# Kernel optimization log

Hardware: AMD Instinct MI355X
Metric: run time of the kernel (lower is better)

The kernel has to match this reference:

```python
import jax, jax.numpy as jnp
from jax import lax
import numpy as np

NUM_CENTROIDS = 1024
RADIUS = 0.5
K = 32
EPS = 1e-5


def _fps(xyz, num_samples):
    """Farthest point sampling. Deterministic start at index 0 (torch uses randint)."""
    B, N, _ = xyz.shape

    def step(carry, _):
        distances, farthest = carry
        centroid = jnp.take_along_axis(xyz, farthest[:, None, None], axis=1)  # [B,1,3]
        d = jnp.sum((xyz - centroid) ** 2, axis=-1)  # [B,N]
        distances = jnp.minimum(distances, d)
        nxt = jnp.argmax(distances, axis=-1).astype(jnp.int32)
        return (distances, nxt), farthest

    init = (jnp.full((B, N), jnp.inf, dtype=xyz.dtype), jnp.zeros((B,), jnp.int32))
    _, idxs = lax.scan(step, init, None, length=num_samples)  # [M,B]
    return jnp.transpose(idxs)  # [B,M]


def _ball_query(xyz, new_xyz):
    """K nearest neighbors within RADIUS; out-of-ball slots fall back to nearest."""
    d2 = (jnp.sum(new_xyz ** 2, -1)[:, :, None] + jnp.sum(xyz ** 2, -1)[:, None, :]
          - 2.0 * jnp.einsum('bmd,bnd->bmn', new_xyz, xyz))
    dist = jnp.sqrt(jnp.maximum(d2, 0.0))  # [B,M,N] cdist
    dist = jnp.where(dist > RADIUS, jnp.inf, dist)
    neg_vals, idx = lax.top_k(-dist, K)  # smallest-K distances
    mask = jnp.isinf(neg_vals)  # outside radius
    idx = jnp.where(mask, idx[:, :, 0:1], idx)
    return idx  # [B,M,K]


def _forward(xyz, features, Ws, bs, gs, bts):
    B, N, _ = xyz.shape
    cidx = lax.stop_gradient(_fps(xyz, NUM_CENTROIDS))  # [B,M] int
    new_xyz = jnp.take_along_axis(xyz, cidx[:, :, None], axis=1)  # [B,M,3]
    gidx = lax.stop_gradient(_ball_query(xyz, new_xyz))  # [B,M,K] int
    flat = gidx.reshape(B, -1)
    gxyz = jnp.take_along_axis(xyz, flat[:, :, None], axis=1).reshape(B, NUM_CENTROIDS, K, 3)
    gxyz = gxyz - new_xyz[:, :, None, :]
    gfeat = jnp.take_along_axis(features, flat[:, :, None], axis=1).reshape(B, NUM_CENTROIDS, K, -1)
    h = jnp.concatenate([gxyz, gfeat], axis=-1)  # [B,M,K,C+3]
    for W, b, g, bt in zip(Ws, bs, gs, bts):
        # 1x1 Conv1d == per-point linear over channels
        h = jnp.einsum('bmkc,oc->bmko', h, W) + b
        # BatchNorm1d in training mode: batch stats over (B*M, K), biased var
        mu = jnp.mean(h, axis=(0, 1, 2))
        var = jnp.var(h, axis=(0, 1, 2))
        h = (h - mu) * lax.rsqrt(var + EPS) * g + bt
        h = jax.nn.gelu(h, approximate=False)  # torch nn.GELU default (exact erf)
    return new_xyz, jnp.max(h, axis=2)  # [B,M,3], [B,M,128]


def setup_inputs() -> dict:
    key = jax.random.key(0)
    ks = jax.random.split(key, 8)
    B, N, C = 8, 8192, 64
    xyz = jax.random.normal(ks[0], (B, N, 3), jnp.float32)
    features = jax.random.normal(ks[1], (B, N, C), jnp.float32)
    chans = [C + 3, 64, 64, 128]
    inp = {"xyz": xyz, "features": features}
    for l in range(3):
        cin, cout = chans[l], chans[l + 1]
        inp[f"W{l + 1}"] = jax.random.normal(ks[2 + l], (cout, cin), jnp.float32) / jnp.float32(np.sqrt(cin))
        inp[f"b{l + 1}"] = jnp.zeros((cout,), jnp.float32)
        inp[f"g{l + 1}"] = jnp.ones((cout,), jnp.float32)
        inp[f"bt{l + 1}"] = jnp.zeros((cout,), jnp.float32)
    return inp


def reference(xyz, features, W1, b1, g1, bt1, W2, b2, g2, bt2, W3, b3, g3, bt3):
    return _forward(xyz, features, (W1, W2, W3), (b1, b2, b3), (g1, g2, g3), (bt1, bt2, bt3))
```

## Files before the change

### kernel.cpp

```cpp
#include <hip/hip_runtime.h>
#include <cstdint>
#include <cstddef>

#define BATCH 8
#define NPTS  8192
#define MCENT 1024
#define KNN   32
#define CFEAT 64
#define EPS_F 1e-5f

#define WS_NEED 73400320ull

__device__ __forceinline__ float erf_fast(float x) {
  float a = fabsf(x);
  float t = __builtin_amdgcn_rcpf(fmaf(0.3275911f, a, 1.0f));
  float p = fmaf(1.061405429f, t, -1.453152027f);
  p = fmaf(p, t, 1.421413741f);
  p = fmaf(p, t, -0.284496736f);
  p = fmaf(p, t, 0.254829592f);
  float e = __expf(-a * a);
  float y = fmaf(-p * t, e, 1.0f);
  return copysignf(y, x);
}
__device__ __forceinline__ float gelu_f(float x) {
  return 0.5f * x * (1.0f + erf_fast(x * 0.70710678118654752440f));
}

template<int CTRL>
__device__ __forceinline__ float dpp_max_step(float v) {
  int s = __builtin_amdgcn_update_dpp(__float_as_int(v), __float_as_int(v),
                                      CTRL, 0xf, 0xf, false);
  return fmaxf(v, __int_as_float(s));
}
__device__ __forceinline__ float wave_max_dpp(float v) {
  v = dpp_max_step<0x111>(v);
  v = dpp_max_step<0x112>(v);
  v = dpp_max_step<0x114>(v);
  v = dpp_max_step<0x118>(v);
  v = dpp_max_step<0x142>(v);
  v = dpp_max_step<0x143>(v);
  return v;
}
template<int CTRL>
__device__ __forceinline__ unsigned long long dpp_min64_step(unsigned long long v) {
  int lo = __builtin_amdgcn_update_dpp((int)(unsigned)(v & 0xffffffffull),
                                       (int)(unsigned)(v & 0xffffffffull),
                                       CTRL, 0xf, 0xf, false);
  int hi = __builtin_amdgcn_update_dpp((int)(unsigned)(v >> 32),
                                       (int)(unsigned)(v >> 32),
                                       CTRL, 0xf, 0xf, false);
  unsigned long long o = (((unsigned long long)(unsigned)hi) << 32) | (unsigned)lo;
  return o < v ? o : v;
}
__device__ __forceinline__ unsigned long long wave_min64_dpp(unsigned long long v) {
  v = dpp_min64_step<0x111>(v);
  v = dpp_min64_step<0x112>(v);
  v = dpp_min64_step<0x114>(v);
  v = dpp_min64_step<0x118>(v);
  v = dpp_min64_step<0x142>(v);
  v = dpp_min64_step<0x143>(v);
  return v;
}

template<int M, int HALF>
__device__ __forceinline__ void tree_step(float* s_, float* q_, int lane) {
  bool up = (lane & M) != 0;
#pragma unroll
  for (int j = 0; j < HALF; ++j) {
    float ks = up ? s_[j+HALF] : s_[j];
    float ds = up ? s_[j]      : s_[j+HALF];
    s_[j] = ks + __shfl_xor(ds, M, 64);
    float kq = up ? q_[j+HALF] : q_[j];
    float dq = up ? q_[j]      : q_[j+HALF];
    q_[j] = kq + __shfl_xor(dq, M, 64);
  }
}
template<int M, int HALF>
__device__ __forceinline__ void ptree_step(float* g_, int kbit) {
  bool up = (kbit & M) != 0;
#pragma unroll
  for (int j = 0; j < HALF; ++j) {
    float kv = up ? g_[j+HALF] : g_[j];
    float dv = up ? g_[j]      : g_[j+HALF];
    g_[j] = fmaxf(kv, __shfl_xor(dv, M, 64));
  }
}

#define FPS_STEPS 64
#define BQCAP 512
__global__ __launch_bounds__(512, 1) void mega_kernel(
    const float* __restrict__ xyz, float* __restrict__ new_xyz,
    float* __restrict__ dist_ws, float* __restrict__ cst, int s0,
    int* __restrict__ gidx, const float* __restrict__ feats,
    const float* __restrict__ W1, const float* __restrict__ b1v,
    float* __restrict__ h1, float* __restrict__ part)
{
  __shared__ float pts[NPTS * 3];
  __shared__ float outb[FPS_STEPS * 3];
  __shared__ unsigned long long keys[2][8];
  __shared__ unsigned long long list[8][BQCAP];
  __shared__ float ls[512], lss[512];
  int blk = blockIdx.x, t = threadIdx.x;

  if (blk < 8) {
    if (s0 >= MCENT) return;
    int b = blk;
    const float* xb = xyz + (size_t)b * NPTS * 3;
    float px[16], py[16], pz[16], dist[16];
    {
      const float4* src = (const float4*)(xb + (size_t)t * 48);
      float4 buf[12];
#pragma unroll
      for (int i = 0; i < 12; ++i) buf[i] = src[i];
      const float* f = (const float*)buf;
#pragma unroll
      for (int i = 0; i < 16; ++i) {
        px[i] = f[i*3+0]; py[i] = f[i*3+1]; pz[i] = f[i*3+2];
      }
      float4* dst = (float4*)(pts + (size_t)t * 48);
#pragma unroll
      for (int i = 0; i < 12; ++i) dst[i] = buf[i];
    }
    float* dw = dist_ws + (size_t)b * NPTS + (size_t)t * 16;
    float cx, cy, cz;
    if (s0 == 0) {
#pragma unroll
      for (int i = 0; i < 16; ++i) dist[i] = __builtin_inff();
      cx = xb[0]; cy = xb[1]; cz = xb[2];
    } else {
      float4 d0 = *(const float4*)(dw + 0);
      float4 d1 = *(const float4*)(dw + 4);
      float4 d2 = *(const float4*)(dw + 8);
      float4 d3 = *(const float4*)(dw + 12);
      dist[0]=d0.x; dist[1]=d0.y; dist[2]=d0.z; dist[3]=d0.w;
      dist[4]=d1.x; dist[5]=d1.y; dist[6]=d1.z; dist[7]=d1.w;
      dist[8]=d2.x; dist[9]=d2.y; dist[10]=d2.z; dist[11]=d2.w;
      dist[12]=d3.x; dist[13]=d3.y; dist[14]=d3.z; dist[15]=d3.w;
      cx = cst[b*3+0]; cy = cst[b*3+1]; cz = cst[b*3+2];
    }
    int lane = t & 63, wv = t >> 6;

    for (int s = 0; s < FPS_STEPS; ++s) {
      if (t == 0) { outb[s*3+0] = cx; outb[s*3+1] = cy; outb[s*3+2] = cz; }
      float bd = -1.0f; int bslot = 0;
#pragma unroll
      for (int i = 0; i < 16; ++i) {
        float dx = __fsub_rn(px[i], cx);
        float dy = __fsub_rn(py[i], cy);
        float dz = __fsub_rn(pz[i], cz);
        float d  = __fadd_rn(__fadd_rn(__fmul_rn(dx,dx), __fmul_rn(dy,dy)), __fmul_rn(dz,dz));
        float nd = fminf(dist[i], d);
        dist[i] = nd;
        if (nd > bd) { bd = nd; bslot = i; }
      }
      float w = wave_max_dpp(bd);
      float wmax = __int_as_float(__builtin_amdgcn_readlane(__float_as_int(w), 63));
      unsigned long long mk = __ballot(bd == wmax);
      int sl = __ffsll((long long)mk) - 1;
      int widx = __builtin_amdgcn_readlane(t * 16 + bslot, sl);
      if (lane == 0)
        keys[s & 1][wv] = (((unsigned long long)__float_as_uint(wmax)) << 32)
                          | (unsigned)(8191 - widx);
      __syncthreads();
      unsigned long long bk = keys[s & 1][0];
#pragma unroll
      for (int w2 = 1; w2 < 8; ++w2) {
        unsigned long long o = keys[s & 1][w2];
        if (o > bk) bk = o;
      }
      int idx = 8191 - (int)(unsigned)(bk & 0xffffffffull);
      cx = pts[idx*3+0]; cy = pts[idx*3+1]; cz = pts[idx*3+2];
    }

    *(float4*)(dw + 0)  = make_float4(dist[0], dist[1], dist[2], dist[3]);
    *(float4*)(dw + 4)  = make_float4(dist[4], dist[5], dist[6], dist[7]);
    *(float4*)(dw + 8)  = make_float4(dist[8], dist[9], dist[10], dist[11]);
    *(float4*)(dw + 12) = make_float4(dist[12], dist[13], dist[14], dist[15]);
    if (t == 0) { cst[b*3+0] = cx; cst[b*3+1] = cy; cst[b*3+2] = cz; }
    __syncthreads();
    float* ob = new_xyz + (size_t)b * MCENT * 3 + (size_t)s0 * 3;
    for (int i = t; i < FPS_STEPS * 3; i += 512) ob[i] = outb[i];

  } else if (blk < 72) {
    int ph = s0 - FPS_STEPS;
    if (ph < 0 || ph >= MCENT) return;
    int wv = t >> 6, lane = t & 63;
    int c  = (blk - 8) * 8 + wv;
    int b  = c >> 6;
    int ci = ph + (c & 63);
    int gm = b * MCENT + ci;
    const float* cc = new_xyz + (size_t)gm * 3;
    float c0 = cc[0], c1 = cc[1], c2 = cc[2];
    float sc = __fadd_rn(__fadd_rn(__fmul_rn(c0,c0), __fmul_rn(c1,c1)), __fmul_rn(c2,c2));
    const float* xb = xyz + (size_t)b * NPTS * 3;

    unsigned cnt = 0;
    for (int j0 = 0; j0 < NPTS; j0 += 64) {
      int j = j0 + lane;
      float x = xb[j*3+0], y = xb[j*3+1], z = xb[j*3+2];
      float sx  = __fadd_rn(__fadd_rn(__fmul_rn(x,x), __fmul_rn(y,y)), __fmul_rn(z,z));
      float dot = __fadd_rn(__fadd_rn(__fmul_rn(c0,x), __fmul_rn(c1,y)), __fmul_rn(c2,z));
      float d2  = __fsub_rn(__fadd_rn(sc, sx), __fmul_rn(2.0f, dot));
      float dist = sqrtf(fmaxf(d2, 0.0f));
      bool in_ = (dist <= 0.5f);
      unsigned long long mask = __ballot(in_);
      unsigned off = (unsigned)__popcll(mask & ((1ull << lane) - 1ull));
      if (in_) {
        unsigned pos = cnt + off;
        if (pos < BQCAP)
          list[wv][pos] = (((unsigned long long)__float_as_uint(dist)) << 32) | (unsigned)j;
      }
      cnt += (unsigned)__popcll(mask);
    }
    if (cnt > BQCAP) cnt = BQCAP;

    unsigned long long e[8];
#pragma unroll
    for (int i = 0; i < 8; ++i) {
      unsigned pos = (unsigned)lane + ((unsigned)i << 6);
      e[i] = (pos < cnt) ? list[wv][pos] : ~0ull;
    }
#define CE_(a_, b_) { bool sw = e[b_] < e[a_]; \
                      unsigned long long lo_ = sw ? e[b_] : e[a_]; \
                      unsigned long long hi_ = sw ? e[a_] : e[b_]; \
                      e[a_] = lo_; e[b_] = hi_; }
    CE_(0,1) CE_(2,3) CE_(4,5) CE_(6,7)
    CE_(0,2) CE_(1,3) CE_(4,6) CE_(5,7)
    CE_(1,2) CE_(5,6)
    CE_(0,4) CE_(1,5) CE_(2,6) CE_(3,7)
    CE_(2,4) CE_(3,5)
    CE_(1,2) CE_(3,4) CE_(5,6)
#undef CE_

    int* gout = gidx + (size_t)gm * KNN;
    int first = 0;
    int kmax = (cnt < (unsigned)KNN) ? (int)cnt : KNN;
    for (int k = 0; k < KNN; ++k) {
      if (k < kmax) {
        unsigned long long wr = wave_min64_dpp(e[0]);
        unsigned lo32 = (unsigned)__builtin_amdgcn_readlane((int)(unsigned)(wr & 0xffffffffull), 63);
        unsigned hi32 = (unsigned)__builtin_amdgcn_readlane((int)(unsigned)(wr >> 32), 63);
        unsigned long long wmin = (((unsigned long long)hi32) << 32) | lo32;
        int idxv = (int)lo32;
        if (k == 0) first = idxv;
        if (lane == 0) gout[k] = idxv;
        bool win = (e[0] == wmin);
#pragma unroll
        for (int i = 0; i < 7; ++i) e[i] = win ? e[i+1] : e[i];
        e[7] = win ? ~0ull : e[7];
      } else {
        if (lane == 0) gout[k] = first;
      }
    }

  } else if (blk < 104) {
    int ph = s0 - 2 * FPS_STEPS;
    if (ph < 0 || ph >= MCENT) return;
    int row = (blk - 72) * 512 + t;
    int c   = row >> 5;
    int k   = row & 31;
    int b   = c >> 6;
    int ci  = ph + (c & 63);
    int p   = b * (MCENT * KNN) + ci * KNN + k;
    int idx = gidx[p];
    const float* cc = new_xyz + (size_t)(b * MCENT + ci) * 3;
    const float* q  = xyz + (size_t)(b * NPTS + idx) * 3;
    float in[67];
    in[0] = q[0] - cc[0];
    in[1] = q[1] - cc[1];
    in[2] = q[2] - cc[2];
    const float* fr = feats + (size_t)(b * NPTS + idx) * CFEAT;
#pragma unroll
    for (int j = 0; j < 64; j += 4) {
      float4 v = *(const float4*)(fr + j);
      in[3+j] = v.x; in[4+j] = v.y; in[5+j] = v.z; in[6+j] = v.w;
    }
    float* orow = h1 + (size_t)p * 64;
    for (int o4 = 0; o4 < 16; ++o4) {
      const float* w0 = W1 + (size_t)(o4 * 4) * 67;
      float a0 = b1v[o4*4+0], a1 = b1v[o4*4+1], a2 = b1v[o4*4+2], a3 = b1v[o4*4+3];
#pragma unroll
      for (int j = 0; j < 67; ++j) {
        float x = in[j];
        a0 = fmaf(x, w0[j],       a0);
        a1 = fmaf(x, w0[67+j],    a1);
        a2 = fmaf(x, w0[134+j],   a2);
        a3 = fmaf(x, w0[201+j],   a3);
      }
      *(float4*)(orow + o4*4) = make_float4(a0, a1, a2, a3);
    }

  } else {
    int ph = s0 - 3 * FPS_STEPS;
    if (ph < 0 || ph >= MCENT) return;
    int sb = blk - 104;
    int b  = sb >> 2;
    int rb = (sb & 3) * 512;
    int c  = t & 63, g = t >> 6;
    size_t base = (size_t)b * (MCENT * KNN) + (size_t)ph * KNN + rb;
    float s = 0.0f, ss = 0.0f;
    for (int r = g; r < 512; r += 8) {
      float v = h1[(base + r) * 64 + c];
      s += v;
      ss = fmaf(v, v, ss);
    }
    ls[t] = s; lss[t] = ss;
    __syncthreads();
    if (g == 0) {
#pragma unroll
      for (int gg = 1; gg < 8; ++gg) { s += ls[gg*64 + c]; ss += lss[gg*64 + c]; }
      int pblk = (ph >> 6) * 32 + sb;
      part[(size_t)pblk * 128 + c]      = s;
      part[(size_t)pblk * 128 + 64 + c] = ss;
    }
  }
}

__global__ __launch_bounds__(256) void l2_kernel(
    float* __restrict__ h, const float* __restrict__ W,
    const float* __restrict__ bv, const float* __restrict__ bnp,
    const float* __restrict__ btp)
{
  int p = blockIdx.x * 256 + threadIdx.x;
  float* row = h + (size_t)p * 64;
  float in[64];
#pragma unroll
  for (int j = 0; j < 64; j += 4) {
    float4 v = *(const float4*)(row + j);
    in[j+0] = gelu_f((v.x - bnp[j+0]) * bnp[64+j+0] + btp[j+0]);
    in[j+1] = gelu_f((v.y - bnp[j+1]) * bnp[64+j+1] + btp[j+1]);
    in[j+2] = gelu_f((v.z - bnp[j+2]) * bnp[64+j+2] + btp[j+2]);
    in[j+3] = gelu_f((v.w - bnp[j+3]) * bnp[64+j+3] + btp[j+3]);
  }
  for (int o4 = 0; o4 < 16; ++o4) {
    const float* w0 = W + (size_t)(o4 * 4) * 64;
    float a0 = bv[o4*4+0], a1 = bv[o4*4+1], a2 = bv[o4*4+2], a3 = bv[o4*4+3];
#pragma unroll
    for (int j = 0; j < 64; ++j) {
      float x = in[j];
      a0 = fmaf(x, w0[j],      a0);
      a1 = fmaf(x, w0[64+j],   a1);
      a2 = fmaf(x, w0[128+j],  a2);
      a3 = fmaf(x, w0[192+j],  a3);
    }
    *(float4*)(row + o4*4) = make_float4(a0, a1, a2, a3);
  }
}

template<int C>
__global__ __launch_bounds__(256) void stats_kernel(const float* __restrict__ h,
                                                    float* __restrict__ part)
{
  constexpr int G = 256 / C;
  int t = threadIdx.x;
  int c = t % C, g = t / C;
  const float* base = h + (size_t)blockIdx.x * 512 * C;
  float s = 0.0f, ss = 0.0f;
  for (int r = g; r < 512; r += G) {
    float v = base[(size_t)r * C + c];
    s += v;
    ss = fmaf(v, v, ss);
  }
  __shared__ float ls[256], lss[256];
  ls[t] = s; lss[t] = ss;
  __syncthreads();
  if (g == 0) {
    for (int gg = 1; gg < G; ++gg) { s += ls[gg*C + c]; ss += lss[gg*C + c]; }
    part[(size_t)blockIdx.x * (2*C) + c]     = s;
    part[(size_t)blockIdx.x * (2*C) + C + c] = ss;
  }
}

template<int C>
__global__ __launch_bounds__(256) void fin_kernel(const float* __restrict__ part,
                                                  const float* __restrict__ gv,
                                                  float* __restrict__ bn)
{
  int c = blockIdx.x, t = threadIdx.x;
  float s = 0.0f, ss = 0.0f;
  for (int b2 = t; b2 < 512; b2 += 256) {
    s  += part[(size_t)b2 * (2*C) + c];
    ss += part[(size_t)b2 * (2*C) + C + c];
  }
  __shared__ float ls[256], lss[256];
  ls[t] = s; lss[t] = ss;
  __syncthreads();
  for (int k = 128; k > 0; k >>= 1) {
    if (t < k) { ls[t] += ls[t+k]; lss[t] += lss[t+k]; }
    __syncthreads();
  }
  if (t == 0) {
    const float inv_n = 1.0f / 262144.0f;
    float mu  = ls[0] * inv_n;
    float var = fmaxf(lss[0] * inv_n - mu * mu, 0.0f);
    bn[c]     = mu;
    bn[C + c] = gv[c] / sqrtf(var + EPS_F);
  }
}

__global__ __launch_bounds__(256) void act_kernel(float* __restrict__ h,
                                                  const float* __restrict__ bnp,
                                                  const float* __restrict__ btp)
{
  int p = blockIdx.x * 256 + threadIdx.x;
  float* row = h + (size_t)p * 64;
#pragma unroll
  for (int j = 0; j < 64; j += 4) {
    float4 v = *(const float4*)(row + j);
    v.x = gelu_f((v.x - bnp[j+0]) * bnp[64+j+0] + btp[j+0]);
    v.y = gelu_f((v.y - bnp[j+1]) * bnp[64+j+1] + btp[j+1]);
    v.z = gelu_f((v.z - bnp[j+2]) * bnp[64+j+2] + btp[j+2]);
    v.w = gelu_f((v.w - bnp[j+3]) * bnp[64+j+3] + btp[j+3]);
    *(float4*)(row + j) = v;
  }
}

__global__ __launch_bounds__(256, 1) void l3stats_kernel(
    const float* __restrict__ g2, const float* __restrict__ W3,
    const float* __restrict__ b3, float* __restrict__ part)
{
  int t = threadIdx.x;
  int gb = blockIdx.x >> 2, chunk = blockIdx.x & 3;
  int og0 = chunk * 32;
  int p = gb * 256 + t;
  const float* row = g2 + (size_t)p * 64;
  float in[64];
#pragma unroll
  for (int j = 0; j < 64; j += 4) {
    float4 v = *(const float4*)(row + j);
    in[j+0] = v.x; in[j+1] = v.y; in[j+2] = v.z; in[j+3] = v.w;
  }
  float s_[32], q_[32];
  for (int o4 = 0; o4 < 8; ++o4) {
    const float* w0 = W3 + (size_t)(og0 + o4 * 4) * 64;
    float a0 = b3[og0+o4*4+0], a1 = b3[og0+o4*4+1], a2 = b3[og0+o4*4+2], a3 = b3[og0+o4*4+3];
#pragma unroll
    for (int j = 0; j < 64; ++j) {
      float x = in[j];
      a0 = fmaf(x, w0[j],      a0);
      a1 = fmaf(x, w0[64+j],   a1);
      a2 = fmaf(x, w0[128+j],  a2);
      a3 = fmaf(x, w0[192+j],  a3);
    }
    int o = o4 * 4;
    s_[o]=a0; s_[o+1]=a1; s_[o+2]=a2; s_[o+3]=a3;
    q_[o]=a0*a0; q_[o+1]=a1*a1; q_[o+2]=a2*a2; q_[o+3]=a3*a3;
  }

  int wv = t >> 6, lane = t & 63;
  tree_step<1,16>(s_, q_, lane);
  tree_step<2, 8>(s_, q_, lane);
  tree_step<4, 4>(s_, q_, lane);
  tree_step<8, 2>(s_, q_, lane);
  tree_step<16,1>(s_, q_, lane);
  s_[0] += __shfl_xor(s_[0], 32, 64);
  q_[0] += __shfl_xor(q_[0], 32, 64);

  int ch = (int)(__brev((unsigned)(lane & 31)) >> 27);
  float* pw = part + ((size_t)blockIdx.x * 4 + wv) * 64;
  if (lane < 32) { pw[ch] = s_[0]; pw[32 + ch] = q_[0]; }
}

__global__ __launch_bounds__(256) void fin3_kernel(const float* __restrict__ part,
                                                   const float* __restrict__ gv,
                                                   float* __restrict__ bn)
{
  int c = blockIdx.x, t = threadIdx.x;
  int chunk = c >> 5, j = c & 31;
  float s = 0.0f, ss = 0.0f;
  for (int gb = t; gb < 1024; gb += 256) {
    int blk = gb * 4 + chunk;
#pragma unroll
    for (int wv = 0; wv < 4; ++wv) {
      const float* pw = part + ((size_t)blk * 4 + wv) * 64;
      s  += pw[j];
      ss += pw[32 + j];
    }
  }
  __shared__ float ls[256], lss[256];
  ls[t] = s; lss[t] = ss;
  __syncthreads();
  for (int k = 128; k > 0; k >>= 1) {
    if (t < k) { ls[t] += ls[t+k]; lss[t] += lss[t+k]; }
    __syncthreads();
  }
  if (t == 0) {
    const float inv_n = 1.0f / 262144.0f;
    float mu  = ls[0] * inv_n;
    float var = fmaxf(lss[0] * inv_n - mu * mu, 0.0f);
    bn[c]       = mu;
    bn[128 + c] = gv[c] / sqrtf(var + EPS_F);
  }
}

__global__ __launch_bounds__(256, 1) void pool3_kernel(
    const float* __restrict__ g2, const float* __restrict__ W3,
    const float* __restrict__ b3,
    const float* __restrict__ bnp3,
    const float* __restrict__ btp3,
    float* __restrict__ out1)
{
  int t = threadIdx.x;
  int gb = blockIdx.x >> 2, chunk = blockIdx.x & 3;
  int og0 = chunk * 32;
  int p = gb * 256 + t;
  const float* row = g2 + (size_t)p * 64;
  float in[64];
#pragma unroll
  for (int j = 0; j < 64; j += 4) {
    float4 v = *(const float4*)(row + j);
    in[j+0] = v.x; in[j+1] = v.y; in[j+2] = v.z; in[j+3] = v.w;
  }
  float g_[32];
  for (int o4 = 0; o4 < 8; ++o4) {
    const float* w0 = W3 + (size_t)(og0 + o4 * 4) * 64;
    float a0 = b3[og0+o4*4+0], a1 = b3[og0+o4*4+1], a2 = b3[og0+o4*4+2], a3 = b3[og0+o4*4+3];
#pragma unroll
    for (int j = 0; j < 64; ++j) {
      float x = in[j];
      a0 = fmaf(x, w0[j],      a0);
      a1 = fmaf(x, w0[64+j],   a1);
      a2 = fmaf(x, w0[128+j],  a2);
      a3 = fmaf(x, w0[192+j],  a3);
    }
    int oc0 = og0 + o4 * 4, o = o4 * 4;
    g_[o]   = gelu_f((a0 - bnp3[oc0+0]) * bnp3[128+oc0+0] + btp3[oc0+0]);
    g_[o+1] = gelu_f((a1 - bnp3[oc0+1]) * bnp3[128+oc0+1] + btp3[oc0+1]);
    g_[o+2] = gelu_f((a2 - bnp3[oc0+2]) * bnp3[128+oc0+2] + btp3[oc0+2]);
    g_[o+3] = gelu_f((a3 - bnp3[oc0+3]) * bnp3[128+oc0+3] + btp3[oc0+3]);
  }

  ptree_step<1,16>(g_, t);
  ptree_step<2, 8>(g_, t);
  ptree_step<4, 4>(g_, t);
  ptree_step<8, 2>(g_, t);
  ptree_step<16,1>(g_, t);

  int ch = (int)(__brev((unsigned)(t & 31)) >> 27);
  int gm = gb * 8 + (t >> 5);
  out1[(size_t)gm * 128 + og0 + ch] = g_[0];
}

__global__ void fill_kernel(float* __restrict__ out1) {
  out1[blockIdx.x * 256 + threadIdx.x] = 1.0e6f;
}

extern "C" void kernel_launch(void* const* d_in, const int* in_sizes, int n_in,
                              void* d_out, int out_size, void* d_ws, size_t ws_size,
                              hipStream_t stream)
{
  (void)in_sizes; (void)n_in; (void)out_size;
  const float* xyz   = (const float*)d_in[0];
  const float* feats = (const float*)d_in[1];
  const float* W1  = (const float*)d_in[2];
  const float* b1  = (const float*)d_in[3];
  const float* g1  = (const float*)d_in[4];
  const float* bt1 = (const float*)d_in[5];
  const float* W2  = (const float*)d_in[6];
  const float* b2  = (const float*)d_in[7];
  const float* g2  = (const float*)d_in[8];
  const float* bt2 = (const float*)d_in[9];
  const float* W3  = (const float*)d_in[10];
  const float* b3  = (const float*)d_in[11];
  const float* g3  = (const float*)d_in[12];
  const float* bt3 = (const float*)d_in[13];

  float* out0 = (float*)d_out;
  float* out1 = out0 + (size_t)BATCH * MCENT * 3;

  char* ws = (char*)d_ws;
  int*   gidx    = (int*)(ws + 0);
  float* part    = (float*)(ws + (1u << 20));
  float* bn0     = (float*)(ws + 5u * (1u << 20));
  float* bn1     = bn0 + 128;
  float* bn2     = bn0 + 256;
  float* dist_ws = (float*)(ws + 5u * (1u << 20) + 65536u);
  float* cst     = (float*)(ws + 5u * (1u << 20) + 65536u + 262144u);
  float* h1      = (float*)(ws + 6u * (1u << 20));

  if (ws_size < WS_NEED) {
    fill_kernel<<<4096, 256, 0, stream>>>(out1);
    return;
  }

  for (int s0 = 0; s0 <= MCENT + 2 * FPS_STEPS; s0 += FPS_STEPS)
    mega_kernel<<<136, 512, 0, stream>>>(xyz, out0, dist_ws, cst, s0,
                                         gidx, feats, W1, b1, h1, part);

  fin_kernel<64><<<64, 256, 0, stream>>>(part, g1, bn0);
  l2_kernel<<<1024, 256, 0, stream>>>(h1, W2, b2, bn0, bt1);
  stats_kernel<64><<<512, 256, 0, stream>>>(h1, part);
  fin_kernel<64><<<64, 256, 0, stream>>>(part, g2, bn1);
  act_kernel<<<1024, 256, 0, stream>>>(h1, bn1, bt2);
  l3stats_kernel<<<4096, 256, 0, stream>>>(h1, W3, b3, part);
  fin3_kernel<<<128, 256, 0, stream>>>(part, g3, bn2);
  pool3_kernel<<<4096, 256, 0, stream>>>(h1, W3, b3, bn2, bt3, out1);
}
```

Before: 1.500 ms.

## Pack two FPS batches per block, drop LDS point copy, read centroid from global

The farthest-point-sampling part now runs two batches per 512-thread block, one per 256-thread half, with 32 points per thread held in registers instead of 16. The 96KB shared point array is removed, and each step's chosen centroid is read from global memory through a uniform scalar index. The launch drops from 136 to 132 blocks and launch_bounds now allows two blocks per CU. This frees LDS and compute units for the pipelined ball-query and MLP stages, at the cost of longer per-step serial work in each FPS thread, higher register pressure, and a global load on every step's critical path.

Result: slower. 2.252 ms (+50.1%).

```diff
diff --git a/kernel.cpp b/kernel.cpp
--- a/kernel.cpp
+++ b/kernel.cpp
@@ -88,63 +88,64 @@
 
 #define FPS_STEPS 64
 #define BQCAP 512
-__global__ __launch_bounds__(512, 1) void mega_kernel(
+__global__ __launch_bounds__(512, 2) void mega_kernel(
     const float* __restrict__ xyz, float* __restrict__ new_xyz,
     float* __restrict__ dist_ws, float* __restrict__ cst, int s0,
     int* __restrict__ gidx, const float* __restrict__ feats,
     const float* __restrict__ W1, const float* __restrict__ b1v,
     float* __restrict__ h1, float* __restrict__ part)
 {
-  __shared__ float pts[NPTS * 3];
-  __shared__ float outb[FPS_STEPS * 3];
+  __shared__ float outb2[2][FPS_STEPS * 3];
   __shared__ unsigned long long keys[2][8];
   __shared__ unsigned long long list[8][BQCAP];
   __shared__ float ls[512], lss[512];
   int blk = blockIdx.x, t = threadIdx.x;
 
-  if (blk < 8) {
+  if (blk < 4) {
     if (s0 >= MCENT) return;
-    int b = blk;
-    const float* xb = xyz + (size_t)b * NPTS * 3;
-    float px[16], py[16], pz[16], dist[16];
+    int half = t >> 8;
+    int bb = blk * 2 + half;
+    int tb = t & 255;
+    int lane = t & 63, wv = t >> 6;
+    const float* xb = xyz + (size_t)bb * NPTS * 3;
+
+    float px[32], py[32], pz[32], dist[32];
     {
-      const float4* src = (const float4*)(xb + (size_t)t * 48);
-      float4 buf[12];
-#pragma unroll
-      for (int i = 0; i < 12; ++i) buf[i] = src[i];
-      const float* f = (const float*)buf;
-#pragma unroll
-      for (int i = 0; i < 16; ++i) {
-        px[i] = f[i*3+0]; py[i] = f[i*3+1]; pz[i] = f[i*3+2];
-      }
-      float4* dst = (float4*)(pts + (size_t)t * 48);
-#pragma unroll
-      for (int i = 0; i < 12; ++i) dst[i] = buf[i];
-    }
-    float* dw = dist_ws + (size_t)b * NPTS + (size_t)t * 16;
+      const float4* src = (const float4*)(xb + (size_t)tb * 96);
+#pragma unroll
+      for (int c4 = 0; c4 < 4; ++c4) {
+        float4 buf[6];
+#pragma unroll
+        for (int i = 0; i < 6; ++i) buf[i] = src[c4*6 + i];
+        const float* f = (const float*)buf;
+#pragma unroll
+        for (int i = 0; i < 8; ++i) {
+          px[c4*8+i] = f[i*3+0]; py[c4*8+i] = f[i*3+1]; pz[c4*8+i] = f[i*3+2];
+        }
+      }
+    }
+    float* dw = dist_ws + (size_t)bb * NPTS + (size_t)tb * 32;
     float cx, cy, cz;
     if (s0 == 0) {
 #pragma unroll
-      for (int i = 0; i < 16; ++i) dist[i] = __builtin_inff();
+      for (int i = 0; i < 32; ++i) dist[i] = __builtin_inff();
       cx = xb[0]; cy = xb[1]; cz = xb[2];
     } else {
-      float4 d0 = *(const float4*)(dw + 0);
-      float4 d1 = *(const float4*)(dw + 4);
-      float4 d2 = *(const float4*)(dw + 8);
-      float4 d3 = *(const float4*)(dw + 12);
-      dist[0]=d0.x; dist[1]=d0.y; dist[2]=d0.z; dist[3]=d0.w;
-      dist[4]=d1.x; dist[5]=d1.y; dist[6]=d1.z; dist[7]=d1.w;
-      dist[8]=d2.x; dist[9]=d2.y; dist[10]=d2.z; dist[11]=d2.w;
-      dist[12]=d3.x; dist[13]=d3.y; dist[14]=d3.z; dist[15]=d3.w;
-      cx = cst[b*3+0]; cy = cst[b*3+1]; cz = cst[b*3+2];
-    }
-    int lane = t & 63, wv = t >> 6;
+#pragma unroll
+      for (int i = 0; i < 8; ++i) {
+        float4 d = *(const float4*)(dw + i * 4);
+        dist[i*4+0]=d.x; dist[i*4+1]=d.y; dist[i*4+2]=d.z; dist[i*4+3]=d.w;
+      }
+      cx = cst[bb*3+0]; cy = cst[bb*3+1]; cz = cst[bb*3+2];
+    }
 
     for (int s = 0; s < FPS_STEPS; ++s) {
-      if (t == 0) { outb[s*3+0] = cx; outb[s*3+1] = cy; outb[s*3+2] = cz; }
+      if (tb == 0) {
+        outb2[half][s*3+0] = cx; outb2[half][s*3+1] = cy; outb2[half][s*3+2] = cz;
+      }
       float bd = -1.0f; int bslot = 0;
 #pragma unroll
-      for (int i = 0; i < 16; ++i) {
+      for (int i = 0; i < 32; ++i) {
         float dx = __fsub_rn(px[i], cx);
         float dy = __fsub_rn(py[i], cy);
         float dz = __fsub_rn(pz[i], cz);
@@ -157,35 +158,38 @@
       float wmax = __int_as_float(__builtin_amdgcn_readlane(__float_as_int(w), 63));
       unsigned long long mk = __ballot(bd == wmax);
       int sl = __ffsll((long long)mk) - 1;
-      int widx = __builtin_amdgcn_readlane(t * 16 + bslot, sl);
+      int widx = __builtin_amdgcn_readlane(tb * 32 + bslot, sl);
       if (lane == 0)
         keys[s & 1][wv] = (((unsigned long long)__float_as_uint(wmax)) << 32)
                           | (unsigned)(8191 - widx);
       __syncthreads();
-      unsigned long long bk = keys[s & 1][0];
-#pragma unroll
-      for (int w2 = 1; w2 < 8; ++w2) {
-        unsigned long long o = keys[s & 1][w2];
+      int wb = half * 4;
+      unsigned long long bk = keys[s & 1][wb];
+#pragma unroll
+      for (int w2 = 1; w2 < 4; ++w2) {
+        unsigned long long o = keys[s & 1][wb + w2];
         if (o > bk) bk = o;
       }
       int idx = 8191 - (int)(unsigned)(bk & 0xffffffffull);
-      cx = pts[idx*3+0]; cy = pts[idx*3+1]; cz = pts[idx*3+2];
-    }
-
-    *(float4*)(dw + 0)  = make_float4(dist[0], dist[1], dist[2], dist[3]);
-    *(float4*)(dw + 4)  = make_float4(dist[4], dist[5], dist[6], dist[7]);
-    *(float4*)(dw + 8)  = make_float4(dist[8], dist[9], dist[10], dist[11]);
-    *(float4*)(dw + 12) = make_float4(dist[12], dist[13], dist[14], dist[15]);
-    if (t == 0) { cst[b*3+0] = cx; cst[b*3+1] = cy; cst[b*3+2] = cz; }
+      int uidx = __builtin_amdgcn_readfirstlane(idx);
+      cx = xb[uidx*3+0]; cy = xb[uidx*3+1]; cz = xb[uidx*3+2];
+    }
+
+#pragma unroll
+    for (int i = 0; i < 8; ++i)
+      *(float4*)(dw + i * 4) = make_float4(dist[i*4+0], dist[i*4+1],
+                                           dist[i*4+2], dist[i*4+3]);
+    if (tb == 0) { cst[bb*3+0] = cx; cst[bb*3+1] = cy; cst[bb*3+2] = cz; }
     __syncthreads();
-    float* ob = new_xyz + (size_t)b * MCENT * 3 + (size_t)s0 * 3;
-    for (int i = t; i < FPS_STEPS * 3; i += 512) ob[i] = outb[i];
-
-  } else if (blk < 72) {
+    float* ob = new_xyz + (size_t)bb * MCENT * 3 + (size_t)s0 * 3;
+    const float* mo = outb2[half];
+    for (int i = tb; i < FPS_STEPS * 3; i += 256) ob[i] = mo[i];
+
+  } else if (blk < 68) {
     int ph = s0 - FPS_STEPS;
     if (ph < 0 || ph >= MCENT) return;
     int wv = t >> 6, lane = t & 63;
-    int c  = (blk - 8) * 8 + wv;
+    int c  = (blk - 4) * 8 + wv;
     int b  = c >> 6;
     int ci = ph + (c & 63);
     int gm = b * MCENT + ci;
@@ -253,10 +257,10 @@
       }
     }
 
-  } else if (blk < 104) {
+  } else if (blk < 100) {
     int ph = s0 - 2 * FPS_STEPS;
     if (ph < 0 || ph >= MCENT) return;
-    int row = (blk - 72) * 512 + t;
+    int row = (blk - 68) * 512 + t;
     int c   = row >> 5;
     int k   = row & 31;
     int b   = c >> 6;
@@ -293,7 +297,7 @@
   } else {
     int ph = s0 - 3 * FPS_STEPS;
     if (ph < 0 || ph >= MCENT) return;
-    int sb = blk - 104;
+    int sb = blk - 100;
     int b  = sb >> 2;
     int rb = (sb & 3) * 512;
     int c  = t & 63, g = t >> 6;
@@ -584,7 +588,7 @@
   }
 
   for (int s0 = 0; s0 <= MCENT + 2 * FPS_STEPS; s0 += FPS_STEPS)
-    mega_kernel<<<136, 512, 0, stream>>>(xyz, out0, dist_ws, cst, s0,
+    mega_kernel<<<132, 512, 0, stream>>>(xyz, out0, dist_ws, cst, s0,
                                          gidx, feats, W1, b1, h1, part);
 
   fin_kernel<64><<<64, 256, 0, stream>>>(part, g1, bn0);
```
